# Performance work log

Hardware: AMD Instinct MI355X
Metric: run time of the kernel (lower is better)

Reference implementation:

```python
import jax, jax.numpy as jnp
import numpy as np

N = 200_000          # nodes
E = 12_800_000       # directed edges (avg degree 64)
C = 5                # channels: [pos_x, pos_y, vel_x, vel_y, extra]
ACCEL_SCALE = 0.01
MAX_VEL = 0.1
MAX_POS = 1.0


def setup_inputs() -> dict:
    key = jax.random.key(0)
    k1, k2, k3 = jax.random.split(key, 3)
    x = jax.random.uniform(k1, (N, C), jnp.float32, -1.0, 1.0)
    edge_index = jax.random.randint(k2, (2, E), 0, N, dtype=jnp.int32)
    # GCNConv learned params (glorot-ish init, zero bias as in PyG)
    W = jax.random.normal(k3, (C, 2), jnp.float32) * (1.0 / np.sqrt(C))
    b = jnp.zeros((2,), jnp.float32)
    return {"x": x, "edge_index": edge_index, "W": W, "b": b, "time_steps": 1}


def _gcn_conv(x, edge_index, W, b):
    """PyG GCNConv: add self-loops, symmetric deg normalization, X @ W, scatter-sum."""
    n = x.shape[0]
    loop = jnp.arange(n, dtype=edge_index.dtype)
    src = jnp.concatenate([edge_index[0], loop])  # [E+N]
    dst = jnp.concatenate([edge_index[1], loop])
    deg = jax.ops.segment_sum(jnp.ones_like(src, x.dtype), dst, num_segments=n)  # [N]
    dinv = jnp.where(deg > 0, jax.lax.rsqrt(deg), 0.0)
    norm = dinv[src] * dinv[dst]                  # [E+N]
    h = x @ W                                     # [N, 2]
    msg = h[src] * norm[:, None]                  # gather + scale, [E+N, 2]
    out = jax.ops.segment_sum(msg, dst, num_segments=n) + b
    return out


def _step(x, edge_index, W, b):
    acc = _gcn_conv(x, edge_index, W, b) * ACCEL_SCALE        # [N, 2]
    vel = jnp.clip(x[:, 2:4] + acc, -MAX_VEL, MAX_VEL)
    pos = jnp.clip(x[:, :2] + vel, -MAX_POS, MAX_POS)
    return jnp.concatenate([pos, vel, x[:, 4:]], axis=1)


def reference(x, edge_index, W, b, time_steps):
    for _ in range(time_steps):
        x = _step(x, edge_index, W, b)
    return x
```

## Files before the change

### kernel.cpp

```cpp
#include <hip/hip_runtime.h>
#include <hip/hip_fp16.h>

constexpr float ACCEL_SCALE = 0.01f;
constexpr float MAX_VEL = 0.1f;
constexpr float MAX_POS = 1.0f;

constexpr int GSHIFT = 11;
constexpr int GSIZE  = 1 << GSHIFT;
constexpr int SCANW  = 128;
constexpr int ANBLK  = 1024;
constexpr int DSHIFT = 4;
constexpr int ASHIFT = 5;

__global__ __launch_bounds__(256) void a_scatter_kernel(
    const int* __restrict__ src, const int* __restrict__ dst,
    int E, int NG, int chunk,
    unsigned* __restrict__ tab, unsigned* __restrict__ packed)
{
    __shared__ int cnt[SCANW];
    __shared__ int tmp[SCANW];
    __shared__ int cur[SCANW];
    int tid = threadIdx.x;
    long long cs64 = (long long)blockIdx.x * chunk;
    int cs = (cs64 > E) ? E : (int)cs64;
    int ce = min(cs + chunk, E);

    if (tid < SCANW) cnt[tid] = 0;
    __syncthreads();

    int nv = (ce - cs) >> 2;
    const int4* d4 = (const int4*)(dst + cs);
    for (int k = tid; k < nv; k += 256) {
        int4 v = d4[k];
        atomicAdd(&cnt[v.x >> GSHIFT], 1);
        atomicAdd(&cnt[v.y >> GSHIFT], 1);
        atomicAdd(&cnt[v.z >> GSHIFT], 1);
        atomicAdd(&cnt[v.w >> GSHIFT], 1);
    }
    for (int i = cs + (nv << 2) + tid; i < ce; i += 256)
        atomicAdd(&cnt[dst[i] >> GSHIFT], 1);
    __syncthreads();

    int v = (tid < SCANW) ? cnt[tid] : 0;
    if (tid < SCANW) tmp[tid] = v;
    __syncthreads();
    for (int off = 1; off < SCANW; off <<= 1) {
        int t = (tid < SCANW && tid >= off) ? tmp[tid - off] : 0;
        __syncthreads();
        if (tid < SCANW) tmp[tid] += t;
        __syncthreads();
    }
    if (tid < SCANW) {
        int base = tmp[tid] - v;
        cur[tid] = base;
        if (tid <= NG) tab[(size_t)blockIdx.x * (NG + 1) + tid] = (unsigned)base;
    }
    __syncthreads();

    const int4* s4 = (const int4*)(src + cs);
    for (int k = tid; k < nv; k += 256) {
        int4 dv = d4[k];
        int4 sv = s4[k];
        int p;
        p = atomicAdd(&cur[dv.x >> GSHIFT], 1);
        packed[cs + p] = ((unsigned)sv.x << GSHIFT) | (unsigned)(dv.x & (GSIZE - 1));
        p = atomicAdd(&cur[dv.y >> GSHIFT], 1);
        packed[cs + p] = ((unsigned)sv.y << GSHIFT) | (unsigned)(dv.y & (GSIZE - 1));
        p = atomicAdd(&cur[dv.z >> GSHIFT], 1);
        packed[cs + p] = ((unsigned)sv.z << GSHIFT) | (unsigned)(dv.z & (GSIZE - 1));
        p = atomicAdd(&cur[dv.w >> GSHIFT], 1);
        packed[cs + p] = ((unsigned)sv.w << GSHIFT) | (unsigned)(dv.w & (GSIZE - 1));
    }
    for (int i = cs + (nv << 2) + tid; i < ce; i += 256) {
        int dvv = dst[i], svv = src[i];
        int p = atomicAdd(&cur[dvv >> GSHIFT], 1);
        packed[cs + p] = ((unsigned)svv << GSHIFT) | (unsigned)(dvv & (GSIZE - 1));
    }
}

__global__ __launch_bounds__(512) void f_deg_kernel(
    const unsigned* __restrict__ packed, const unsigned* __restrict__ tab,
    int E, int NG, int chunk, int n, int splitShift, int* __restrict__ pdeg)
{
    __shared__ int cnt[GSIZE];
    int g = blockIdx.x >> splitShift;
    int s = blockIdx.x & ((1 << splitShift) - 1);
    for (int t = threadIdx.x; t < GSIZE; t += 512) cnt[t] = 0;
    __syncthreads();
    int wave = threadIdx.x >> 6, lane = threadIdx.x & 63;
    int perSplit = ANBLK >> splitShift;
    int j0 = s * perSplit, jend = j0 + perSplit;
    int j = j0 + wave;
    unsigned nt0 = 0, nt1 = 0;
    if (j < jend) { const unsigned* tr = tab + (size_t)j * (NG + 1) + g; nt0 = tr[0]; nt1 = tr[1]; }
    for (; j < jend; j += 8) {
        unsigned t0 = nt0, t1 = nt1;
        int jn = j + 8;
        if (jn < jend) { const unsigned* tr = tab + (size_t)jn * (NG + 1) + g; nt0 = tr[0]; nt1 = tr[1]; }
        long long cs64 = (long long)j * chunk;
        int cs = (cs64 > E) ? E : (int)cs64;
        for (unsigned i = t0 + lane; i < t1; i += 64)
            atomicAdd(&cnt[packed[cs + i] & (GSIZE - 1)], 1);
    }
    __syncthreads();
    size_t nb0 = (size_t)g << GSHIFT;
    for (int t = threadIdx.x; t < GSIZE; t += 512) {
        size_t node = nb0 + t;
        if (node < (size_t)n) pdeg[(size_t)s * n + node] = cnt[t];
    }
}

__global__ void node_preh_kernel(const float* __restrict__ x, const float* __restrict__ W,
                                 const int* __restrict__ pdeg, int n, int nsplit,
                                 float* __restrict__ dinv, __half2* __restrict__ hsh) {
    int i = blockIdx.x * blockDim.x + threadIdx.x;
    if (i >= n) return;
    int d = 1;
    for (int s = 0; s < nsplit; ++s) d += pdeg[(size_t)s * n + i];
    float di = rsqrtf((float)d);
    dinv[i] = di;
    const float* xr = x + (size_t)i * 5;
    float x0 = xr[0], x1 = xr[1], x2 = xr[2], x3 = xr[3], x4 = xr[4];
    float h0 = x0 * W[0] + x1 * W[2] + x2 * W[4] + x3 * W[6] + x4 * W[8];
    float h1 = x0 * W[1] + x1 * W[3] + x2 * W[5] + x3 * W[7] + x4 * W[9];
    hsh[i] = __floats2half2_rn(h0 * di, h1 * di);
}

__global__ __launch_bounds__(512) void a_acc5_kernel(
    const unsigned* __restrict__ packed, const unsigned* __restrict__ tab,
    const __half2* __restrict__ hsh, int E, int NG, int chunk, int n,
    __half2* __restrict__ psh)
{
    __shared__ __half2 acc[GSIZE];
    int g = blockIdx.x >> ASHIFT;
    int s = blockIdx.x & ((1 << ASHIFT) - 1);
    const __half2 zero = __floats2half2_rn(0.f, 0.f);
    for (int t = threadIdx.x; t < GSIZE; t += 512) acc[t] = zero;
    __syncthreads();
    int wave = threadIdx.x >> 6, lane = threadIdx.x & 63;
    const int perSplit = ANBLK >> ASHIFT;
    int j0 = s * perSplit, jend = j0 + perSplit;
    int j = j0 + wave;
    unsigned nt0 = 0, nt1 = 0;
    if (j < jend) { const unsigned* tr = tab + (size_t)j * (NG + 1) + g; nt0 = tr[0]; nt1 = tr[1]; }
    for (; j < jend; j += 8) {
        unsigned t0 = nt0, t1 = nt1;
        int jn = j + 8;
        if (jn < jend) { const unsigned* tr = tab + (size_t)jn * (NG + 1) + g; nt0 = tr[0]; nt1 = tr[1]; }
        long long cs64 = (long long)j * chunk;
        int cs = (cs64 > E) ? E : (int)cs64;
        for (unsigned i = t0 + lane; i < t1; i += 64) {
            unsigned p = packed[cs + i];
            __half2 m = hsh[p >> GSHIFT];
            unsafeAtomicAdd(&acc[p & (GSIZE - 1)], m);
        }
    }
    __syncthreads();
    size_t nb0 = (size_t)g << GSHIFT;
    for (int t = threadIdx.x; t < GSIZE; t += 512) {
        size_t node = nb0 + t;
        if (node < (size_t)n) psh[(size_t)s * n + node] = acc[t];
    }
}

__global__ void a_finalh_kernel(const float* __restrict__ x, const __half2* __restrict__ psh,
                                const float* __restrict__ W, const float* __restrict__ dinv,
                                const float* __restrict__ b, float* __restrict__ out,
                                int n, int nsplit) {
    int i = blockIdx.x * blockDim.x + threadIdx.x;
    if (i >= n) return;
    float sx = 0.f, sy = 0.f;
    for (int s = 0; s < nsplit; ++s) {
        float2 v = __half22float2(psh[(size_t)s * n + i]);
        sx += v.x; sy += v.y;
    }
    float di = dinv[i];
    const float* xr = x + (size_t)i * 5;
    float x0 = xr[0], x1 = xr[1], x2 = xr[2], x3 = xr[3], x4 = xr[4];
    float h0 = x0 * W[0] + x1 * W[2] + x2 * W[4] + x3 * W[6] + x4 * W[8];
    float h1 = x0 * W[1] + x1 * W[3] + x2 * W[5] + x3 * W[7] + x4 * W[9];
    float c0 = di * (sx + h0 * di) + b[0];
    float c1 = di * (sy + h1 * di) + b[1];
    float a0 = c0 * ACCEL_SCALE;
    float a1 = c1 * ACCEL_SCALE;
    float v0 = fminf(fmaxf(x2 + a0, -MAX_VEL), MAX_VEL);
    float v1 = fminf(fmaxf(x3 + a1, -MAX_VEL), MAX_VEL);
    float p0 = fminf(fmaxf(x0 + v0, -MAX_POS), MAX_POS);
    float p1 = fminf(fmaxf(x1 + v1, -MAX_POS), MAX_POS);
    float* o = out + (size_t)i * 5;
    o[0] = p0; o[1] = p1; o[2] = v0; o[3] = v1; o[4] = x4;
}

__global__ void node_pre_kernel(const float* __restrict__ x, const float* __restrict__ W,
                                const int* __restrict__ pdeg, int n, int nsplit,
                                float* __restrict__ dinv, float* __restrict__ hs) {
    int i = blockIdx.x * blockDim.x + threadIdx.x;
    if (i >= n) return;
    int d = 1;
    for (int s = 0; s < nsplit; ++s) d += pdeg[(size_t)s * n + i];
    float di = rsqrtf((float)d);
    dinv[i] = di;
    const float* xr = x + (size_t)i * 5;
    float x0 = xr[0], x1 = xr[1], x2 = xr[2], x3 = xr[3], x4 = xr[4];
    float h0 = x0 * W[0] + x1 * W[2] + x2 * W[4] + x3 * W[6] + x4 * W[8];
    float h1 = x0 * W[1] + x1 * W[3] + x2 * W[5] + x3 * W[7] + x4 * W[9];
    hs[2 * i]     = h0 * di;
    hs[2 * i + 1] = h1 * di;
}

__global__ __launch_bounds__(512) void f_acc_kernel(
    const unsigned* __restrict__ packed, const unsigned* __restrict__ tab,
    const float* __restrict__ hs, int E, int NG, int chunk, int n, int splitShift,
    float2* __restrict__ ps)
{
    __shared__ float accx[GSIZE];
    __shared__ float accy[GSIZE];
    int g = blockIdx.x >> splitShift;
    int s = blockIdx.x & ((1 << splitShift) - 1);
    for (int t = threadIdx.x; t < GSIZE; t += 512) { accx[t] = 0.f; accy[t] = 0.f; }
    __syncthreads();
    int wave = threadIdx.x >> 6, lane = threadIdx.x & 63;
    int perSplit = ANBLK >> splitShift;
    int j0 = s * perSplit, jend = j0 + perSplit;
    const float2* h2 = (const float2*)hs;
    int j = j0 + wave;
    unsigned nt0 = 0, nt1 = 0;
    if (j < jend) { const unsigned* tr = tab + (size_t)j * (NG + 1) + g; nt0 = tr[0]; nt1 = tr[1]; }
    for (; j < jend; j += 8) {
        unsigned t0 = nt0, t1 = nt1;
        int jn = j + 8;
        if (jn < jend) { const unsigned* tr = tab + (size_t)jn * (NG + 1) + g; nt0 = tr[0]; nt1 = tr[1]; }
        long long cs64 = (long long)j * chunk;
        int cs = (cs64 > E) ? E : (int)cs64;
        for (unsigned i = t0 + lane; i < t1; i += 64) {
            unsigned p = packed[cs + i];
            float2 m = h2[p >> GSHIFT];
            int ld = p & (GSIZE - 1);
            unsafeAtomicAdd(&accx[ld], m.x);
            unsafeAtomicAdd(&accy[ld], m.y);
        }
    }
    __syncthreads();
    size_t nb0 = (size_t)g << GSHIFT;
    for (int t = threadIdx.x; t < GSIZE; t += 512) {
        size_t node = nb0 + t;
        if (node < (size_t)n) ps[(size_t)s * n + node] = make_float2(accx[t], accy[t]);
    }
}

__global__ void a_final_kernel(const float* __restrict__ x, const float2* __restrict__ ps,
                               const float* __restrict__ hs, const float* __restrict__ dinv,
                               const float* __restrict__ b, float* __restrict__ out,
                               int n, int nsplit) {
    int i = blockIdx.x * blockDim.x + threadIdx.x;
    if (i >= n) return;
    float sx = 0.f, sy = 0.f;
    for (int s = 0; s < nsplit; ++s) {
        float2 v = ps[(size_t)s * n + i];
        sx += v.x; sy += v.y;
    }
    const float2* h2 = (const float2*)hs;
    float di = dinv[i];
    float2 hv = h2[i];
    float c0 = di * (sx + hv.x) + b[0];
    float c1 = di * (sy + hv.y) + b[1];
    float a0 = c0 * ACCEL_SCALE;
    float a1 = c1 * ACCEL_SCALE;
    const float* xr = x + (size_t)i * 5;
    float v0 = fminf(fmaxf(xr[2] + a0, -MAX_VEL), MAX_VEL);
    float v1 = fminf(fmaxf(xr[3] + a1, -MAX_VEL), MAX_VEL);
    float p0 = fminf(fmaxf(xr[0] + v0, -MAX_POS), MAX_POS);
    float p1 = fminf(fmaxf(xr[1] + v1, -MAX_POS), MAX_POS);
    float* o = out + (size_t)i * 5;
    o[0] = p0; o[1] = p1; o[2] = v0; o[3] = v1; o[4] = xr[4];
}

__global__ void fb_deg_kernel(const int* __restrict__ dst, int E, int* __restrict__ deg) {
    int tid = blockIdx.x * blockDim.x + threadIdx.x;
    int stride = gridDim.x * blockDim.x;
    for (int k = tid; k < E; k += stride) atomicAdd(&deg[dst[k]], 1);
}
__global__ void fb_scatter_kernel(const int* __restrict__ src, const int* __restrict__ dst,
                                  int E, const float* __restrict__ hs, float* __restrict__ s) {
    int tid = blockIdx.x * blockDim.x + threadIdx.x;
    int stride = gridDim.x * blockDim.x;
    const float2* h2 = (const float2*)hs;
    for (int k = tid; k < E; k += stride) {
        int sv = src[k], dv = dst[k];
        float2 m = h2[sv];
        unsafeAtomicAdd(&s[2 * dv], m.x);
        unsafeAtomicAdd(&s[2 * dv + 1], m.y);
    }
}
__global__ void fb_np_kernel(const float* __restrict__ x, const float* __restrict__ W,
                             const int* __restrict__ deg, int n,
                             float* __restrict__ dinv, float* __restrict__ hs) {
    int i = blockIdx.x * blockDim.x + threadIdx.x;
    if (i >= n) return;
    float di = rsqrtf((float)(deg[i] + 1));
    dinv[i] = di;
    const float* xr = x + (size_t)i * 5;
    float x0 = xr[0], x1 = xr[1], x2 = xr[2], x3 = xr[3], x4 = xr[4];
    float h0 = x0 * W[0] + x1 * W[2] + x2 * W[4] + x3 * W[6] + x4 * W[8];
    float h1 = x0 * W[1] + x1 * W[3] + x2 * W[5] + x3 * W[7] + x4 * W[9];
    hs[2 * i] = h0 * di;
    hs[2 * i + 1] = h1 * di;
}
__global__ void fb_finalize_kernel(const float* __restrict__ x, const float* __restrict__ s,
                                   const float* __restrict__ hs, const float* __restrict__ dinv,
                                   const float* __restrict__ b, float* __restrict__ out, int n) {
    int i = blockIdx.x * blockDim.x + threadIdx.x;
    if (i >= n) return;
    float di = dinv[i];
    const float2* s2 = (const float2*)s;
    const float2* h2 = (const float2*)hs;
    float2 sv = s2[i];
    float2 hv = h2[i];
    float c0 = di * (sv.x + hv.x) + b[0];
    float c1 = di * (sv.y + hv.y) + b[1];
    float a0 = c0 * ACCEL_SCALE, a1 = c1 * ACCEL_SCALE;
    const float* xr = x + (size_t)i * 5;
    float v0 = fminf(fmaxf(xr[2] + a0, -MAX_VEL), MAX_VEL);
    float v1 = fminf(fmaxf(xr[3] + a1, -MAX_VEL), MAX_VEL);
    float p0 = fminf(fmaxf(xr[0] + v0, -MAX_POS), MAX_POS);
    float p1 = fminf(fmaxf(xr[1] + v1, -MAX_POS), MAX_POS);
    float* o = out + (size_t)i * 5;
    o[0] = p0; o[1] = p1; o[2] = v0; o[3] = v1; o[4] = xr[4];
}

extern "C" void kernel_launch(void* const* d_in, const int* in_sizes, int n_in,
                              void* d_out, int out_size, void* d_ws, size_t ws_size,
                              hipStream_t stream) {
    const float* x    = (const float*)d_in[0];
    const int*   edge = (const int*)d_in[1];
    const float* W    = (const float*)d_in[2];
    const float* b    = (const float*)d_in[3];

    int n = in_sizes[0] / 5;
    int E = in_sizes[1] / 2;
    const int* src = edge;
    const int* dst = edge + E;

    const int BLK = 256;
    int node_blocks = (n + BLK - 1) / BLK;
    int NG = (n + GSIZE - 1) >> GSHIFT;
    int chunk = ((E + ANBLK - 1) / ANBLK + 3) & ~3;
    bool geomOK = (NG >= 1) && (NG + 1 <= SCANW) && (n <= (1 << 21)) && (E >= 8);

    if (geomOK) {
        const int dsplit = 1 << DSHIFT;
        const int asplit = 1 << ASHIFT;
        size_t wTab = (size_t)ANBLK * (NG + 1);
        size_t needW = (size_t)E + wTab + (size_t)dsplit * n + (size_t)asplit * n
                     + (size_t)n + (size_t)n;
        if (ws_size >= needW * 4) {
            unsigned* packed = (unsigned*)d_ws;
            unsigned* tab    = packed + E;
            int*      pdeg   = (int*)(tab + wTab);
            __half2*  psh    = (__half2*)(pdeg + (size_t)dsplit * n);
            float*    dinv   = (float*)(psh + (size_t)asplit * n);
            __half2*  hsh    = (__half2*)(dinv + n);

            a_scatter_kernel<<<ANBLK, 256, 0, stream>>>(src, dst, E, NG, chunk, tab, packed);
            f_deg_kernel<<<NG << DSHIFT, 512, 0, stream>>>(packed, tab, E, NG, chunk, n,
                                                           DSHIFT, pdeg);
            node_preh_kernel<<<node_blocks, BLK, 0, stream>>>(x, W, pdeg, n, dsplit, dinv, hsh);
            a_acc5_kernel<<<NG << ASHIFT, 512, 0, stream>>>(packed, tab, hsh, E, NG, chunk, n,
                                                            psh);
            a_finalh_kernel<<<node_blocks, BLK, 0, stream>>>(x, psh, W, dinv, b,
                                                             (float*)d_out, n, asplit);
            return;
        }
    }

    if (geomOK) {
        size_t baseW = (size_t)E + (size_t)ANBLK * (NG + 1) + (size_t)n + 2 * (size_t)n;
        size_t needF = (baseW + (size_t)4 * n * 2) * 4;
        if (ws_size >= needF) {
            const int splitShift = 2, split = 4;
            unsigned* packed = (unsigned*)d_ws;
            unsigned* tab    = packed + E;
            int* region      = (int*)(tab + (size_t)ANBLK * (NG + 1));
            int* pdeg        = region;
            float2* ps       = (float2*)region;
            float* dinv      = (float*)(region + (size_t)split * n * 2);
            float* hs        = dinv + n;

            a_scatter_kernel<<<ANBLK, 256, 0, stream>>>(src, dst, E, NG, chunk, tab, packed);
            f_deg_kernel<<<NG << splitShift, 512, 0, stream>>>(packed, tab, E, NG, chunk, n,
                                                               splitShift, pdeg);
            node_pre_kernel<<<node_blocks, BLK, 0, stream>>>(x, W, pdeg, n, split, dinv, hs);
            f_acc_kernel<<<NG << splitShift, 512, 0, stream>>>(packed, tab, hs, E, NG, chunk, n,
                                                               splitShift, ps);
            a_final_kernel<<<node_blocks, BLK, 0, stream>>>(x, ps, hs, dinv, b,
                                                            (float*)d_out, n, split);
            return;
        }
    }

    {
        float* dinv = (float*)d_ws;
        float* hs   = dinv + n;
        float* s    = hs + 2 * (size_t)n;
        int*   deg  = (int*)(s + 2 * (size_t)n);
        hipMemsetAsync(deg, 0, (size_t)n * sizeof(int), stream);
        hipMemsetAsync(s,   0, (size_t)n * 2 * sizeof(float), stream);
        fb_deg_kernel<<<4096, BLK, 0, stream>>>(dst, E, deg);
        fb_np_kernel<<<node_blocks, BLK, 0, stream>>>(x, W, deg, n, dinv, hs);
        fb_scatter_kernel<<<4096, BLK, 0, stream>>>(src, dst, E, hs, s);
        fb_finalize_kernel<<<node_blocks, BLK, 0, stream>>>(x, s, hs, dinv, b, (float*)d_out, n);
    }
}
```

Measured before the change: 173.9 us.

## Replace two-pass count-scan bucketing with single-pass fixed-capacity bins plus overflow list

The edge bucketing kernel no longer counts, scans and then scatters. Each block writes edges straight into fixed-capacity per-(block,group) slots, using a shared atomic cursor, and spills any excess into a global overflow list. Later kernels fix up the spilled edges with global atomics. This removes one full pass over the edge arrays and the scan, at the cost of a padded workspace, extra small kernels and a memset, and the overflow list is capped and silently drops edges past that cap.

New measurement: 178.9 us. 2.9% more time.

```diff
diff --git a/kernel.cpp b/kernel.cpp
--- a/kernel.cpp
+++ b/kernel.cpp
@@ -11,6 +11,190 @@
 constexpr int ANBLK  = 1024;
 constexpr int DSHIFT = 4;
 constexpr int ASHIFT = 5;
+constexpr int CAP    = 176;
+constexpr int OCAP   = 262144;
+
+
+__global__ __launch_bounds__(256) void n_scatter_kernel(
+    const int* __restrict__ src, const int* __restrict__ dst,
+    int E, int NG, int chunk,
+    unsigned* __restrict__ tabc, unsigned* __restrict__ packed,
+    unsigned* __restrict__ gofl, int2* __restrict__ ofl)
+{
+    __shared__ int cur[SCANW];
+    int tid = threadIdx.x;
+    long long cs64 = (long long)blockIdx.x * chunk;
+    int cs = (cs64 > E) ? E : (int)cs64;
+    int ce = min(cs + chunk, E);
+    if (tid < SCANW) cur[tid] = 0;
+    __syncthreads();
+
+    size_t obase = (size_t)blockIdx.x * NG;
+    int nv = (ce - cs) >> 2;
+    const int4* d4 = (const int4*)(dst + cs);
+    const int4* s4 = (const int4*)(src + cs);
+
+#define PROC(dd, ss)                                                            \
+    {                                                                           \
+        int b_ = (dd) >> GSHIFT;                                                \
+        int p_ = atomicAdd(&cur[b_], 1);                                        \
+        unsigned w_ = ((unsigned)(ss) << GSHIFT) | (unsigned)((dd) & (GSIZE-1));\
+        if (p_ < CAP) {                                                         \
+            packed[(obase + b_) * (size_t)CAP + p_] = w_;                       \
+        } else {                                                                \
+            unsigned op_ = atomicAdd(gofl, 1u);                                 \
+            if (op_ < (unsigned)OCAP) ofl[op_] = make_int2((ss), (dd));         \
+        }                                                                       \
+    }
+
+    for (int k = tid; k < nv; k += 256) {
+        int4 dv = d4[k];
+        int4 sv = s4[k];
+        PROC(dv.x, sv.x)
+        PROC(dv.y, sv.y)
+        PROC(dv.z, sv.z)
+        PROC(dv.w, sv.w)
+    }
+    for (int i = cs + (nv << 2) + tid; i < ce; i += 256) {
+        int dd = dst[i], ss = src[i];
+        PROC(dd, ss)
+    }
+#undef PROC
+    __syncthreads();
+    if (tid < NG) tabc[obase + tid] = (unsigned)min(cur[tid], CAP);
+}
+
+__global__ __launch_bounds__(512) void n_deg_kernel(
+    const unsigned* __restrict__ packed, const unsigned* __restrict__ tabc,
+    int NG, int n, int* __restrict__ pdeg)
+{
+    __shared__ int cnt[GSIZE];
+    int g = blockIdx.x >> DSHIFT;
+    int s = blockIdx.x & ((1 << DSHIFT) - 1);
+    for (int t = threadIdx.x; t < GSIZE; t += 512) cnt[t] = 0;
+    __syncthreads();
+    int wave = threadIdx.x >> 6, lane = threadIdx.x & 63;
+    const int perSplit = ANBLK >> DSHIFT;
+    int j0 = s * perSplit, jend = j0 + perSplit;
+    int j = j0 + wave;
+    unsigned nc = 0;
+    if (j < jend) nc = tabc[(size_t)j * NG + g];
+    for (; j < jend; j += 8) {
+        unsigned c = nc;
+        int jn = j + 8;
+        if (jn < jend) nc = tabc[(size_t)jn * NG + g];
+        size_t base = ((size_t)j * NG + g) * (size_t)CAP;
+        for (unsigned i = lane; i < c; i += 64)
+            atomicAdd(&cnt[packed[base + i] & (GSIZE - 1)], 1);
+    }
+    __syncthreads();
+    size_t nb0 = (size_t)g << GSHIFT;
+    for (int t = threadIdx.x; t < GSIZE; t += 512) {
+        size_t node = nb0 + t;
+        if (node < (size_t)n) pdeg[(size_t)s * n + node] = cnt[t];
+    }
+}
+
+__global__ void cln_deg_kernel(const unsigned* __restrict__ gofl, const int2* __restrict__ ofl,
+                               int* __restrict__ pdeg) {
+    unsigned oc = *gofl;
+    if (oc > (unsigned)OCAP) oc = OCAP;
+    for (unsigned k = blockIdx.x * blockDim.x + threadIdx.x; k < oc;
+         k += blockDim.x * gridDim.x)
+        atomicAdd(&pdeg[ofl[k].y], 1);
+}
+
+__global__ void node_preh_kernel(const float* __restrict__ x, const float* __restrict__ W,
+                                 const int* __restrict__ pdeg, int n, int nsplit,
+                                 float* __restrict__ dinv, __half2* __restrict__ hsh) {
+    int i = blockIdx.x * blockDim.x + threadIdx.x;
+    if (i >= n) return;
+    int d = 1;
+    for (int s = 0; s < nsplit; ++s) d += pdeg[(size_t)s * n + i];
+    float di = rsqrtf((float)d);
+    dinv[i] = di;
+    const float* xr = x + (size_t)i * 5;
+    float x0 = xr[0], x1 = xr[1], x2 = xr[2], x3 = xr[3], x4 = xr[4];
+    float h0 = x0 * W[0] + x1 * W[2] + x2 * W[4] + x3 * W[6] + x4 * W[8];
+    float h1 = x0 * W[1] + x1 * W[3] + x2 * W[5] + x3 * W[7] + x4 * W[9];
+    hsh[i] = __floats2half2_rn(h0 * di, h1 * di);
+}
+
+__global__ __launch_bounds__(512) void n_acc_kernel(
+    const unsigned* __restrict__ packed, const unsigned* __restrict__ tabc,
+    const __half2* __restrict__ hsh, int NG, int n,
+    __half2* __restrict__ psh)
+{
+    __shared__ __half2 acc[GSIZE];
+    int g = blockIdx.x >> ASHIFT;
+    int s = blockIdx.x & ((1 << ASHIFT) - 1);
+    const __half2 zero = __floats2half2_rn(0.f, 0.f);
+    for (int t = threadIdx.x; t < GSIZE; t += 512) acc[t] = zero;
+    __syncthreads();
+    int wave = threadIdx.x >> 6, lane = threadIdx.x & 63;
+    const int perSplit = ANBLK >> ASHIFT;
+    int j0 = s * perSplit, jend = j0 + perSplit;
+    int j = j0 + wave;
+    unsigned nc = 0;
+    if (j < jend) nc = tabc[(size_t)j * NG + g];
+    for (; j < jend; j += 8) {
+        unsigned c = nc;
+        int jn = j + 8;
+        if (jn < jend) nc = tabc[(size_t)jn * NG + g];
+        size_t base = ((size_t)j * NG + g) * (size_t)CAP;
+        for (unsigned i = lane; i < c; i += 64) {
+            unsigned p = packed[base + i];
+            __half2 m = hsh[p >> GSHIFT];
+            unsafeAtomicAdd(&acc[p & (GSIZE - 1)], m);
+        }
+    }
+    __syncthreads();
+    size_t nb0 = (size_t)g << GSHIFT;
+    for (int t = threadIdx.x; t < GSIZE; t += 512) {
+        size_t node = nb0 + t;
+        if (node < (size_t)n) psh[(size_t)s * n + node] = acc[t];
+    }
+}
+
+__global__ void cln_acc_kernel(const unsigned* __restrict__ gofl, const int2* __restrict__ ofl,
+                               const __half2* __restrict__ hsh, __half2* __restrict__ psh) {
+    unsigned oc = *gofl;
+    if (oc > (unsigned)OCAP) oc = OCAP;
+    for (unsigned k = blockIdx.x * blockDim.x + threadIdx.x; k < oc;
+         k += blockDim.x * gridDim.x) {
+        int2 e = ofl[k];
+        unsafeAtomicAdd(&psh[e.y], hsh[e.x]);
+    }
+}
+
+__global__ void a_finalh_kernel(const float* __restrict__ x, const __half2* __restrict__ psh,
+                                const float* __restrict__ W, const float* __restrict__ dinv,
+                                const float* __restrict__ b, float* __restrict__ out,
+                                int n, int nsplit) {
+    int i = blockIdx.x * blockDim.x + threadIdx.x;
+    if (i >= n) return;
+    float sx = 0.f, sy = 0.f;
+    for (int s = 0; s < nsplit; ++s) {
+        float2 v = __half22float2(psh[(size_t)s * n + i]);
+        sx += v.x; sy += v.y;
+    }
+    float di = dinv[i];
+    const float* xr = x + (size_t)i * 5;
+    float x0 = xr[0], x1 = xr[1], x2 = xr[2], x3 = xr[3], x4 = xr[4];
+    float h0 = x0 * W[0] + x1 * W[2] + x2 * W[4] + x3 * W[6] + x4 * W[8];
+    float h1 = x0 * W[1] + x1 * W[3] + x2 * W[5] + x3 * W[7] + x4 * W[9];
+    float c0 = di * (sx + h0 * di) + b[0];
+    float c1 = di * (sy + h1 * di) + b[1];
+    float a0 = c0 * ACCEL_SCALE;
+    float a1 = c1 * ACCEL_SCALE;
+    float v0 = fminf(fmaxf(x2 + a0, -MAX_VEL), MAX_VEL);
+    float v1 = fminf(fmaxf(x3 + a1, -MAX_VEL), MAX_VEL);
+    float p0 = fminf(fmaxf(x0 + v0, -MAX_POS), MAX_POS);
+    float p1 = fminf(fmaxf(x1 + v1, -MAX_POS), MAX_POS);
+    float* o = out + (size_t)i * 5;
+    o[0] = p0; o[1] = p1; o[2] = v0; o[3] = v1; o[4] = x4;
+}
+
 
 __global__ __launch_bounds__(256) void a_scatter_kernel(
     const int* __restrict__ src, const int* __restrict__ dst,
@@ -108,22 +292,6 @@
         size_t node = nb0 + t;
         if (node < (size_t)n) pdeg[(size_t)s * n + node] = cnt[t];
     }
-}
-
-__global__ void node_preh_kernel(const float* __restrict__ x, const float* __restrict__ W,
-                                 const int* __restrict__ pdeg, int n, int nsplit,
-                                 float* __restrict__ dinv, __half2* __restrict__ hsh) {
-    int i = blockIdx.x * blockDim.x + threadIdx.x;
-    if (i >= n) return;
-    int d = 1;
-    for (int s = 0; s < nsplit; ++s) d += pdeg[(size_t)s * n + i];
-    float di = rsqrtf((float)d);
-    dinv[i] = di;
-    const float* xr = x + (size_t)i * 5;
-    float x0 = xr[0], x1 = xr[1], x2 = xr[2], x3 = xr[3], x4 = xr[4];
-    float h0 = x0 * W[0] + x1 * W[2] + x2 * W[4] + x3 * W[6] + x4 * W[8];
-    float h1 = x0 * W[1] + x1 * W[3] + x2 * W[5] + x3 * W[7] + x4 * W[9];
-    hsh[i] = __floats2half2_rn(h0 * di, h1 * di);
 }
 
 __global__ __launch_bounds__(512) void a_acc5_kernel(
@@ -161,118 +329,6 @@
         size_t node = nb0 + t;
         if (node < (size_t)n) psh[(size_t)s * n + node] = acc[t];
     }
-}
-
-__global__ void a_finalh_kernel(const float* __restrict__ x, const __half2* __restrict__ psh,
-                                const float* __restrict__ W, const float* __restrict__ dinv,
-                                const float* __restrict__ b, float* __restrict__ out,
-                                int n, int nsplit) {
-    int i = blockIdx.x * blockDim.x + threadIdx.x;
-    if (i >= n) return;
-    float sx = 0.f, sy = 0.f;
-    for (int s = 0; s < nsplit; ++s) {
-        float2 v = __half22float2(psh[(size_t)s * n + i]);
-        sx += v.x; sy += v.y;
-    }
-    float di = dinv[i];
-    const float* xr = x + (size_t)i * 5;
-    float x0 = xr[0], x1 = xr[1], x2 = xr[2], x3 = xr[3], x4 = xr[4];
-    float h0 = x0 * W[0] + x1 * W[2] + x2 * W[4] + x3 * W[6] + x4 * W[8];
-    float h1 = x0 * W[1] + x1 * W[3] + x2 * W[5] + x3 * W[7] + x4 * W[9];
-    float c0 = di * (sx + h0 * di) + b[0];
-    float c1 = di * (sy + h1 * di) + b[1];
-    float a0 = c0 * ACCEL_SCALE;
-    float a1 = c1 * ACCEL_SCALE;
-    float v0 = fminf(fmaxf(x2 + a0, -MAX_VEL), MAX_VEL);
-    float v1 = fminf(fmaxf(x3 + a1, -MAX_VEL), MAX_VEL);
-    float p0 = fminf(fmaxf(x0 + v0, -MAX_POS), MAX_POS);
-    float p1 = fminf(fmaxf(x1 + v1, -MAX_POS), MAX_POS);
-    float* o = out + (size_t)i * 5;
-    o[0] = p0; o[1] = p1; o[2] = v0; o[3] = v1; o[4] = x4;
-}
-
-__global__ void node_pre_kernel(const float* __restrict__ x, const float* __restrict__ W,
-                                const int* __restrict__ pdeg, int n, int nsplit,
-                                float* __restrict__ dinv, float* __restrict__ hs) {
-    int i = blockIdx.x * blockDim.x + threadIdx.x;
-    if (i >= n) return;
-    int d = 1;
-    for (int s = 0; s < nsplit; ++s) d += pdeg[(size_t)s * n + i];
-    float di = rsqrtf((float)d);
-    dinv[i] = di;
-    const float* xr = x + (size_t)i * 5;
-    float x0 = xr[0], x1 = xr[1], x2 = xr[2], x3 = xr[3], x4 = xr[4];
-    float h0 = x0 * W[0] + x1 * W[2] + x2 * W[4] + x3 * W[6] + x4 * W[8];
-    float h1 = x0 * W[1] + x1 * W[3] + x2 * W[5] + x3 * W[7] + x4 * W[9];
-    hs[2 * i]     = h0 * di;
-    hs[2 * i + 1] = h1 * di;
-}
-
-__global__ __launch_bounds__(512) void f_acc_kernel(
-    const unsigned* __restrict__ packed, const unsigned* __restrict__ tab,
-    const float* __restrict__ hs, int E, int NG, int chunk, int n, int splitShift,
-    float2* __restrict__ ps)
-{
-    __shared__ float accx[GSIZE];
-    __shared__ float accy[GSIZE];
-    int g = blockIdx.x >> splitShift;
-    int s = blockIdx.x & ((1 << splitShift) - 1);
-    for (int t = threadIdx.x; t < GSIZE; t += 512) { accx[t] = 0.f; accy[t] = 0.f; }
-    __syncthreads();
-    int wave = threadIdx.x >> 6, lane = threadIdx.x & 63;
-    int perSplit = ANBLK >> splitShift;
-    int j0 = s * perSplit, jend = j0 + perSplit;
-    const float2* h2 = (const float2*)hs;
-    int j = j0 + wave;
-    unsigned nt0 = 0, nt1 = 0;
-    if (j < jend) { const unsigned* tr = tab + (size_t)j * (NG + 1) + g; nt0 = tr[0]; nt1 = tr[1]; }
-    for (; j < jend; j += 8) {
-        unsigned t0 = nt0, t1 = nt1;
-        int jn = j + 8;
-        if (jn < jend) { const unsigned* tr = tab + (size_t)jn * (NG + 1) + g; nt0 = tr[0]; nt1 = tr[1]; }
-        long long cs64 = (long long)j * chunk;
-        int cs = (cs64 > E) ? E : (int)cs64;
-        for (unsigned i = t0 + lane; i < t1; i += 64) {
-            unsigned p = packed[cs + i];
-            float2 m = h2[p >> GSHIFT];
-            int ld = p & (GSIZE - 1);
-            unsafeAtomicAdd(&accx[ld], m.x);
-            unsafeAtomicAdd(&accy[ld], m.y);
-        }
-    }
-    __syncthreads();
-    size_t nb0 = (size_t)g << GSHIFT;
-    for (int t = threadIdx.x; t < GSIZE; t += 512) {
-        size_t node = nb0 + t;
-        if (node < (size_t)n) ps[(size_t)s * n + node] = make_float2(accx[t], accy[t]);
-    }
-}
-
-__global__ void a_final_kernel(const float* __restrict__ x, const float2* __restrict__ ps,
-                               const float* __restrict__ hs, const float* __restrict__ dinv,
-                               const float* __restrict__ b, float* __restrict__ out,
-                               int n, int nsplit) {
-    int i = blockIdx.x * blockDim.x + threadIdx.x;
-    if (i >= n) return;
-    float sx = 0.f, sy = 0.f;
-    for (int s = 0; s < nsplit; ++s) {
-        float2 v = ps[(size_t)s * n + i];
-        sx += v.x; sy += v.y;
-    }
-    const float2* h2 = (const float2*)hs;
-    float di = dinv[i];
-    float2 hv = h2[i];
-    float c0 = di * (sx + hv.x) + b[0];
-    float c1 = di * (sy + hv.y) + b[1];
-    float a0 = c0 * ACCEL_SCALE;
-    float a1 = c1 * ACCEL_SCALE;
-    const float* xr = x + (size_t)i * 5;
-    float v0 = fminf(fmaxf(xr[2] + a0, -MAX_VEL), MAX_VEL);
-    float v1 = fminf(fmaxf(xr[3] + a1, -MAX_VEL), MAX_VEL);
-    float p0 = fminf(fmaxf(xr[0] + v0, -MAX_POS), MAX_POS);
-    float p1 = fminf(fmaxf(xr[1] + v1, -MAX_POS), MAX_POS);
-    float* o = out + (size_t)i * 5;
-    o[0] = p0; o[1] = p1; o[2] = v0; o[3] = v1; o[4] = xr[4];
 }
 
 __global__ void fb_deg_kernel(const int* __restrict__ dst, int E, int* __restrict__ deg) {
@@ -345,15 +401,44 @@
     int node_blocks = (n + BLK - 1) / BLK;
     int NG = (n + GSIZE - 1) >> GSHIFT;
     int chunk = ((E + ANBLK - 1) / ANBLK + 3) & ~3;
-    bool geomOK = (NG >= 1) && (NG + 1 <= SCANW) && (n <= (1 << 21)) && (E >= 8);
-
-    if (geomOK) {
-        const int dsplit = 1 << DSHIFT;
-        const int asplit = 1 << ASHIFT;
+    const int dsplit = 1 << DSHIFT;
+    const int asplit = 1 << ASHIFT;
+    bool geomOK = (NG >= 1) && (NG <= SCANW) && (n <= (1 << 21)) && (E >= 8);
+
+    if (geomOK && NG + 1 <= SCANW) {
+        size_t cells = (size_t)ANBLK * NG;
+        size_t needN = 16 + cells * CAP + cells + (size_t)2 * OCAP
+                     + (size_t)asplit * n + (size_t)n + (size_t)n;
+        if (ws_size >= needN * 4) {
+            unsigned* gofl   = (unsigned*)d_ws;
+            unsigned* packed = gofl + 16;
+            unsigned* tabc   = packed + cells * CAP;
+            int2*     ofl    = (int2*)(tabc + cells);
+            int*      region = (int*)(ofl + OCAP);
+            int*      pdeg   = region;
+            __half2*  psh    = (__half2*)region;
+            float*    dinv   = (float*)(region + (size_t)asplit * n);
+            __half2*  hsh    = (__half2*)(dinv + n);
+
+            hipMemsetAsync(gofl, 0, 64, stream);
+            n_scatter_kernel<<<ANBLK, 256, 0, stream>>>(src, dst, E, NG, chunk,
+                                                        tabc, packed, gofl, ofl);
+            n_deg_kernel<<<NG << DSHIFT, 512, 0, stream>>>(packed, tabc, NG, n, pdeg);
+            cln_deg_kernel<<<4, 256, 0, stream>>>(gofl, ofl, pdeg);
+            node_preh_kernel<<<node_blocks, BLK, 0, stream>>>(x, W, pdeg, n, dsplit, dinv, hsh);
+            n_acc_kernel<<<NG << ASHIFT, 512, 0, stream>>>(packed, tabc, hsh, NG, n, psh);
+            cln_acc_kernel<<<4, 256, 0, stream>>>(gofl, ofl, hsh, psh);
+            a_finalh_kernel<<<node_blocks, BLK, 0, stream>>>(x, psh, W, dinv, b,
+                                                             (float*)d_out, n, asplit);
+            return;
+        }
+    }
+
+    if (geomOK && NG + 1 <= SCANW) {
         size_t wTab = (size_t)ANBLK * (NG + 1);
-        size_t needW = (size_t)E + wTab + (size_t)dsplit * n + (size_t)asplit * n
+        size_t needF = (size_t)E + wTab + (size_t)dsplit * n + (size_t)asplit * n
                      + (size_t)n + (size_t)n;
-        if (ws_size >= needW * 4) {
+        if (ws_size >= needF * 4) {
             unsigned* packed = (unsigned*)d_ws;
             unsigned* tab    = packed + E;
             int*      pdeg   = (int*)(tab + wTab);
@@ -369,31 +454,6 @@
                                                             psh);
             a_finalh_kernel<<<node_blocks, BLK, 0, stream>>>(x, psh, W, dinv, b,
                                                              (float*)d_out, n, asplit);
-            return;
-        }
-    }
-
-    if (geomOK) {
-        size_t baseW = (size_t)E + (size_t)ANBLK * (NG + 1) + (size_t)n + 2 * (size_t)n;
-        size_t needF = (baseW + (size_t)4 * n * 2) * 4;
-        if (ws_size >= needF) {
-            const int splitShift = 2, split = 4;
-            unsigned* packed = (unsigned*)d_ws;
-            unsigned* tab    = packed + E;
-            int* region      = (int*)(tab + (size_t)ANBLK * (NG + 1));
-            int* pdeg        = region;
-            float2* ps       = (float2*)region;
-            float* dinv      = (float*)(region + (size_t)split * n * 2);
-            float* hs        = dinv + n;
-
-            a_scatter_kernel<<<ANBLK, 256, 0, stream>>>(src, dst, E, NG, chunk, tab, packed);
-            f_deg_kernel<<<NG << splitShift, 512, 0, stream>>>(packed, tab, E, NG, chunk, n,
-                                                               splitShift, pdeg);
-            node_pre_kernel<<<node_blocks, BLK, 0, stream>>>(x, W, pdeg, n, split, dinv, hs);
-            f_acc_kernel<<<NG << splitShift, 512, 0, stream>>>(packed, tab, hs, E, NG, chunk, n,
-                                                               splitShift, ps);
-            a_final_kernel<<<node_blocks, BLK, 0, stream>>>(x, ps, hs, dinv, b,
-                                                            (float*)d_out, n, split);
             return;
         }
     }
```

## Replace shared atomic bucket counting with per-thread histograms and deterministic scan

Applied to the files above, without the earlier changes.

Adds a partition kernel in which each thread keeps its own 16-bit bucket counters in LDS, replacing shared-memory atomics during both the counting and the placement passes. Per-bucket prefix sums over the thread histograms give each thread fixed write offsets, so placement within a chunk becomes deterministic and atomic-free. The cost is a large LDS footprint (about 50KB) that limits occupancy, a serial 128-step scan per bucket, and loss of int4-vectorised loads. The older fp32 fallback path is removed and the original scatter is kept only when the group count exceeds the padding.

Measured after the change: 294.4 us. 1.69x slower.

```diff
diff --git a/kernel.cpp b/kernel.cpp
--- a/kernel.cpp
+++ b/kernel.cpp
@@ -8,41 +8,55 @@
 constexpr int GSHIFT = 11;
 constexpr int GSIZE  = 1 << GSHIFT;
 constexpr int SCANW  = 128;
+constexpr int BPAD   = 100;
 constexpr int ANBLK  = 1024;
 constexpr int DSHIFT = 4;
 constexpr int ASHIFT = 5;
 
-__global__ __launch_bounds__(256) void a_scatter_kernel(
+
+__global__ __launch_bounds__(256) void p_scatter_kernel(
     const int* __restrict__ src, const int* __restrict__ dst,
     int E, int NG, int chunk,
     unsigned* __restrict__ tab, unsigned* __restrict__ packed)
 {
-    __shared__ int cnt[SCANW];
+    __shared__ unsigned short cnt[256][BPAD];
+    __shared__ unsigned halfTot[BPAD][2];
+    __shared__ int bbase[SCANW];
     __shared__ int tmp[SCANW];
-    __shared__ int cur[SCANW];
     int tid = threadIdx.x;
     long long cs64 = (long long)blockIdx.x * chunk;
     int cs = (cs64 > E) ? E : (int)cs64;
     int ce = min(cs + chunk, E);
-
-    if (tid < SCANW) cnt[tid] = 0;
-    __syncthreads();
-
-    int nv = (ce - cs) >> 2;
-    const int4* d4 = (const int4*)(dst + cs);
-    for (int k = tid; k < nv; k += 256) {
-        int4 v = d4[k];
-        atomicAdd(&cnt[v.x >> GSHIFT], 1);
-        atomicAdd(&cnt[v.y >> GSHIFT], 1);
-        atomicAdd(&cnt[v.z >> GSHIFT], 1);
-        atomicAdd(&cnt[v.w >> GSHIFT], 1);
-    }
-    for (int i = cs + (nv << 2) + tid; i < ce; i += 256)
-        atomicAdd(&cnt[dst[i] >> GSHIFT], 1);
-    __syncthreads();
-
-    int v = (tid < SCANW) ? cnt[tid] : 0;
-    if (tid < SCANW) tmp[tid] = v;
+    int len = ce - cs;
+
+    unsigned* cz = (unsigned*)&cnt[0][0];
+    for (int i = tid; i < 256 * BPAD / 2; i += 256) cz[i] = 0;
+    __syncthreads();
+
+    for (int k = tid; k < len; k += 256) {
+        int b = dst[cs + k] >> GSHIFT;
+        cnt[tid][b] = (unsigned short)(cnt[tid][b] + 1);
+    }
+    __syncthreads();
+
+    if (tid < 2 * NG) {
+        int b = tid >> 1, half = tid & 1;
+        int t0 = half << 7;
+        unsigned run = 0;
+        for (int i = 0; i < 128; ++i) {
+            unsigned v = cnt[t0 + i][b];
+            cnt[t0 + i][b] = (unsigned short)run;
+            run += v;
+        }
+        halfTot[b][half] = run;
+    }
+    __syncthreads();
+
+    int v = 0;
+    if (tid < SCANW) {
+        v = (tid < NG) ? (int)(halfTot[tid][0] + halfTot[tid][1]) : 0;
+        tmp[tid] = v;
+    }
     __syncthreads();
     for (int off = 1; off < SCANW; off <<= 1) {
         int t = (tid < SCANW && tid >= off) ? tmp[tid - off] : 0;
@@ -52,29 +66,18 @@
     }
     if (tid < SCANW) {
         int base = tmp[tid] - v;
-        cur[tid] = base;
+        bbase[tid] = base;
         if (tid <= NG) tab[(size_t)blockIdx.x * (NG + 1) + tid] = (unsigned)base;
     }
     __syncthreads();
 
-    const int4* s4 = (const int4*)(src + cs);
-    for (int k = tid; k < nv; k += 256) {
-        int4 dv = d4[k];
-        int4 sv = s4[k];
-        int p;
-        p = atomicAdd(&cur[dv.x >> GSHIFT], 1);
-        packed[cs + p] = ((unsigned)sv.x << GSHIFT) | (unsigned)(dv.x & (GSIZE - 1));
-        p = atomicAdd(&cur[dv.y >> GSHIFT], 1);
-        packed[cs + p] = ((unsigned)sv.y << GSHIFT) | (unsigned)(dv.y & (GSIZE - 1));
-        p = atomicAdd(&cur[dv.z >> GSHIFT], 1);
-        packed[cs + p] = ((unsigned)sv.z << GSHIFT) | (unsigned)(dv.z & (GSIZE - 1));
-        p = atomicAdd(&cur[dv.w >> GSHIFT], 1);
-        packed[cs + p] = ((unsigned)sv.w << GSHIFT) | (unsigned)(dv.w & (GSIZE - 1));
-    }
-    for (int i = cs + (nv << 2) + tid; i < ce; i += 256) {
-        int dvv = dst[i], svv = src[i];
-        int p = atomicAdd(&cur[dvv >> GSHIFT], 1);
-        packed[cs + p] = ((unsigned)svv << GSHIFT) | (unsigned)(dvv & (GSIZE - 1));
+    for (int k = tid; k < len; k += 256) {
+        int dd = dst[cs + k], ss = src[cs + k];
+        int b = dd >> GSHIFT;
+        unsigned r = cnt[tid][b];
+        cnt[tid][b] = (unsigned short)(r + 1);
+        int p = bbase[b] + (int)r + (int)((tid >> 7) ? halfTot[b][0] : 0u);
+        packed[cs + p] = ((unsigned)ss << GSHIFT) | (unsigned)(dd & (GSIZE - 1));
     }
 }
 
@@ -191,88 +194,71 @@
     o[0] = p0; o[1] = p1; o[2] = v0; o[3] = v1; o[4] = x4;
 }
 
-__global__ void node_pre_kernel(const float* __restrict__ x, const float* __restrict__ W,
-                                const int* __restrict__ pdeg, int n, int nsplit,
-                                float* __restrict__ dinv, float* __restrict__ hs) {
-    int i = blockIdx.x * blockDim.x + threadIdx.x;
-    if (i >= n) return;
-    int d = 1;
-    for (int s = 0; s < nsplit; ++s) d += pdeg[(size_t)s * n + i];
-    float di = rsqrtf((float)d);
-    dinv[i] = di;
-    const float* xr = x + (size_t)i * 5;
-    float x0 = xr[0], x1 = xr[1], x2 = xr[2], x3 = xr[3], x4 = xr[4];
-    float h0 = x0 * W[0] + x1 * W[2] + x2 * W[4] + x3 * W[6] + x4 * W[8];
-    float h1 = x0 * W[1] + x1 * W[3] + x2 * W[5] + x3 * W[7] + x4 * W[9];
-    hs[2 * i]     = h0 * di;
-    hs[2 * i + 1] = h1 * di;
-}
-
-__global__ __launch_bounds__(512) void f_acc_kernel(
-    const unsigned* __restrict__ packed, const unsigned* __restrict__ tab,
-    const float* __restrict__ hs, int E, int NG, int chunk, int n, int splitShift,
-    float2* __restrict__ ps)
+
+__global__ __launch_bounds__(256) void a_scatter_kernel(
+    const int* __restrict__ src, const int* __restrict__ dst,
+    int E, int NG, int chunk,
+    unsigned* __restrict__ tab, unsigned* __restrict__ packed)
 {
-    __shared__ float accx[GSIZE];
-    __shared__ float accy[GSIZE];
-    int g = blockIdx.x >> splitShift;
-    int s = blockIdx.x & ((1 << splitShift) - 1);
-    for (int t = threadIdx.x; t < GSIZE; t += 512) { accx[t] = 0.f; accy[t] = 0.f; }
-    __syncthreads();
-    int wave = threadIdx.x >> 6, lane = threadIdx.x & 63;
-    int perSplit = ANBLK >> splitShift;
-    int j0 = s * perSplit, jend = j0 + perSplit;
-    const float2* h2 = (const float2*)hs;
-    int j = j0 + wave;
-    unsigned nt0 = 0, nt1 = 0;
-    if (j < jend) { const unsigned* tr = tab + (size_t)j * (NG + 1) + g; nt0 = tr[0]; nt1 = tr[1]; }
-    for (; j < jend; j += 8) {
-        unsigned t0 = nt0, t1 = nt1;
-        int jn = j + 8;
-        if (jn < jend) { const unsigned* tr = tab + (size_t)jn * (NG + 1) + g; nt0 = tr[0]; nt1 = tr[1]; }
-        long long cs64 = (long long)j * chunk;
-        int cs = (cs64 > E) ? E : (int)cs64;
-        for (unsigned i = t0 + lane; i < t1; i += 64) {
-            unsigned p = packed[cs + i];
-            float2 m = h2[p >> GSHIFT];
-            int ld = p & (GSIZE - 1);
-            unsafeAtomicAdd(&accx[ld], m.x);
-            unsafeAtomicAdd(&accy[ld], m.y);
-        }
-    }
-    __syncthreads();
-    size_t nb0 = (size_t)g << GSHIFT;
-    for (int t = threadIdx.x; t < GSIZE; t += 512) {
-        size_t node = nb0 + t;
-        if (node < (size_t)n) ps[(size_t)s * n + node] = make_float2(accx[t], accy[t]);
-    }
-}
-
-__global__ void a_final_kernel(const float* __restrict__ x, const float2* __restrict__ ps,
-                               const float* __restrict__ hs, const float* __restrict__ dinv,
-                               const float* __restrict__ b, float* __restrict__ out,
-                               int n, int nsplit) {
-    int i = blockIdx.x * blockDim.x + threadIdx.x;
-    if (i >= n) return;
-    float sx = 0.f, sy = 0.f;
-    for (int s = 0; s < nsplit; ++s) {
-        float2 v = ps[(size_t)s * n + i];
-        sx += v.x; sy += v.y;
-    }
-    const float2* h2 = (const float2*)hs;
-    float di = dinv[i];
-    float2 hv = h2[i];
-    float c0 = di * (sx + hv.x) + b[0];
-    float c1 = di * (sy + hv.y) + b[1];
-    float a0 = c0 * ACCEL_SCALE;
-    float a1 = c1 * ACCEL_SCALE;
-    const float* xr = x + (size_t)i * 5;
-    float v0 = fminf(fmaxf(xr[2] + a0, -MAX_VEL), MAX_VEL);
-    float v1 = fminf(fmaxf(xr[3] + a1, -MAX_VEL), MAX_VEL);
-    float p0 = fminf(fmaxf(xr[0] + v0, -MAX_POS), MAX_POS);
-    float p1 = fminf(fmaxf(xr[1] + v1, -MAX_POS), MAX_POS);
-    float* o = out + (size_t)i * 5;
-    o[0] = p0; o[1] = p1; o[2] = v0; o[3] = v1; o[4] = xr[4];
+    __shared__ int cnt[SCANW];
+    __shared__ int tmp[SCANW];
+    __shared__ int cur[SCANW];
+    int tid = threadIdx.x;
+    long long cs64 = (long long)blockIdx.x * chunk;
+    int cs = (cs64 > E) ? E : (int)cs64;
+    int ce = min(cs + chunk, E);
+
+    if (tid < SCANW) cnt[tid] = 0;
+    __syncthreads();
+
+    int nv = (ce - cs) >> 2;
+    const int4* d4 = (const int4*)(dst + cs);
+    for (int k = tid; k < nv; k += 256) {
+        int4 v = d4[k];
+        atomicAdd(&cnt[v.x >> GSHIFT], 1);
+        atomicAdd(&cnt[v.y >> GSHIFT], 1);
+        atomicAdd(&cnt[v.z >> GSHIFT], 1);
+        atomicAdd(&cnt[v.w >> GSHIFT], 1);
+    }
+    for (int i = cs + (nv << 2) + tid; i < ce; i += 256)
+        atomicAdd(&cnt[dst[i] >> GSHIFT], 1);
+    __syncthreads();
+
+    int v = (tid < SCANW) ? cnt[tid] : 0;
+    if (tid < SCANW) tmp[tid] = v;
+    __syncthreads();
+    for (int off = 1; off < SCANW; off <<= 1) {
+        int t = (tid < SCANW && tid >= off) ? tmp[tid - off] : 0;
+        __syncthreads();
+        if (tid < SCANW) tmp[tid] += t;
+        __syncthreads();
+    }
+    if (tid < SCANW) {
+        int base = tmp[tid] - v;
+        cur[tid] = base;
+        if (tid <= NG) tab[(size_t)blockIdx.x * (NG + 1) + tid] = (unsigned)base;
+    }
+    __syncthreads();
+
+    const int4* s4 = (const int4*)(src + cs);
+    for (int k = tid; k < nv; k += 256) {
+        int4 dv = d4[k];
+        int4 sv = s4[k];
+        int p;
+        p = atomicAdd(&cur[dv.x >> GSHIFT], 1);
+        packed[cs + p] = ((unsigned)sv.x << GSHIFT) | (unsigned)(dv.x & (GSIZE - 1));
+        p = atomicAdd(&cur[dv.y >> GSHIFT], 1);
+        packed[cs + p] = ((unsigned)sv.y << GSHIFT) | (unsigned)(dv.y & (GSIZE - 1));
+        p = atomicAdd(&cur[dv.z >> GSHIFT], 1);
+        packed[cs + p] = ((unsigned)sv.z << GSHIFT) | (unsigned)(dv.z & (GSIZE - 1));
+        p = atomicAdd(&cur[dv.w >> GSHIFT], 1);
+        packed[cs + p] = ((unsigned)sv.w << GSHIFT) | (unsigned)(dv.w & (GSIZE - 1));
+    }
+    for (int i = cs + (nv << 2) + tid; i < ce; i += 256) {
+        int dvv = dst[i], svv = src[i];
+        int p = atomicAdd(&cur[dvv >> GSHIFT], 1);
+        packed[cs + p] = ((unsigned)svv << GSHIFT) | (unsigned)(dvv & (GSIZE - 1));
+    }
 }
 
 __global__ void fb_deg_kernel(const int* __restrict__ dst, int E, int* __restrict__ deg) {
@@ -345,57 +331,50 @@
     int node_blocks = (n + BLK - 1) / BLK;
     int NG = (n + GSIZE - 1) >> GSHIFT;
     int chunk = ((E + ANBLK - 1) / ANBLK + 3) & ~3;
+    const int dsplit = 1 << DSHIFT;
+    const int asplit = 1 << ASHIFT;
     bool geomOK = (NG >= 1) && (NG + 1 <= SCANW) && (n <= (1 << 21)) && (E >= 8);
 
-    if (geomOK) {
-        const int dsplit = 1 << DSHIFT;
-        const int asplit = 1 << ASHIFT;
-        size_t wTab = (size_t)ANBLK * (NG + 1);
-        size_t needW = (size_t)E + wTab + (size_t)dsplit * n + (size_t)asplit * n
-                     + (size_t)n + (size_t)n;
-        if (ws_size >= needW * 4) {
-            unsigned* packed = (unsigned*)d_ws;
-            unsigned* tab    = packed + E;
-            int*      pdeg   = (int*)(tab + wTab);
-            __half2*  psh    = (__half2*)(pdeg + (size_t)dsplit * n);
-            float*    dinv   = (float*)(psh + (size_t)asplit * n);
-            __half2*  hsh    = (__half2*)(dinv + n);
-
-            a_scatter_kernel<<<ANBLK, 256, 0, stream>>>(src, dst, E, NG, chunk, tab, packed);
-            f_deg_kernel<<<NG << DSHIFT, 512, 0, stream>>>(packed, tab, E, NG, chunk, n,
-                                                           DSHIFT, pdeg);
-            node_preh_kernel<<<node_blocks, BLK, 0, stream>>>(x, W, pdeg, n, dsplit, dinv, hsh);
-            a_acc5_kernel<<<NG << ASHIFT, 512, 0, stream>>>(packed, tab, hsh, E, NG, chunk, n,
-                                                            psh);
-            a_finalh_kernel<<<node_blocks, BLK, 0, stream>>>(x, psh, W, dinv, b,
-                                                             (float*)d_out, n, asplit);
-            return;
-        }
-    }
-
-    if (geomOK) {
-        size_t baseW = (size_t)E + (size_t)ANBLK * (NG + 1) + (size_t)n + 2 * (size_t)n;
-        size_t needF = (baseW + (size_t)4 * n * 2) * 4;
-        if (ws_size >= needF) {
-            const int splitShift = 2, split = 4;
-            unsigned* packed = (unsigned*)d_ws;
-            unsigned* tab    = packed + E;
-            int* region      = (int*)(tab + (size_t)ANBLK * (NG + 1));
-            int* pdeg        = region;
-            float2* ps       = (float2*)region;
-            float* dinv      = (float*)(region + (size_t)split * n * 2);
-            float* hs        = dinv + n;
-
-            a_scatter_kernel<<<ANBLK, 256, 0, stream>>>(src, dst, E, NG, chunk, tab, packed);
-            f_deg_kernel<<<NG << splitShift, 512, 0, stream>>>(packed, tab, E, NG, chunk, n,
-                                                               splitShift, pdeg);
-            node_pre_kernel<<<node_blocks, BLK, 0, stream>>>(x, W, pdeg, n, split, dinv, hs);
-            f_acc_kernel<<<NG << splitShift, 512, 0, stream>>>(packed, tab, hs, E, NG, chunk, n,
-                                                               splitShift, ps);
-            a_final_kernel<<<node_blocks, BLK, 0, stream>>>(x, ps, hs, dinv, b,
-                                                            (float*)d_out, n, split);
-            return;
-        }
+    size_t wTab = (size_t)ANBLK * (NG + 1);
+    size_t needW = (size_t)E + wTab + (size_t)dsplit * n + (size_t)asplit * n
+                 + (size_t)n + (size_t)n;
+
+    if (geomOK && NG <= BPAD && ws_size >= needW * 4) {
+        unsigned* packed = (unsigned*)d_ws;
+        unsigned* tab    = packed + E;
+        int*      pdeg   = (int*)(tab + wTab);
+        __half2*  psh    = (__half2*)(pdeg + (size_t)dsplit * n);
+        float*    dinv   = (float*)(psh + (size_t)asplit * n);
+        __half2*  hsh    = (__half2*)(dinv + n);
+
+        p_scatter_kernel<<<ANBLK, 256, 0, stream>>>(src, dst, E, NG, chunk, tab, packed);
+        f_deg_kernel<<<NG << DSHIFT, 512, 0, stream>>>(packed, tab, E, NG, chunk, n,
+                                                       DSHIFT, pdeg);
+        node_preh_kernel<<<node_blocks, BLK, 0, stream>>>(x, W, pdeg, n, dsplit, dinv, hsh);
+        a_acc5_kernel<<<NG << ASHIFT, 512, 0, stream>>>(packed, tab, hsh, E, NG, chunk, n,
+                                                        psh);
+        a_finalh_kernel<<<node_blocks, BLK, 0, stream>>>(x, psh, W, dinv, b,
+                                                         (float*)d_out, n, asplit);
+        return;
+    }
+
+    if (geomOK && ws_size >= needW * 4) {
+        unsigned* packed = (unsigned*)d_ws;
+        unsigned* tab    = packed + E;
+        int*      pdeg   = (int*)(tab + wTab);
+        __half2*  psh    = (__half2*)(pdeg + (size_t)dsplit * n);
+        float*    dinv   = (float*)(psh + (size_t)asplit * n);
+        __half2*  hsh    = (__half2*)(dinv + n);
+
+        a_scatter_kernel<<<ANBLK, 256, 0, stream>>>(src, dst, E, NG, chunk, tab, packed);
+        f_deg_kernel<<<NG << DSHIFT, 512, 0, stream>>>(packed, tab, E, NG, chunk, n,
+                                                       DSHIFT, pdeg);
+        node_preh_kernel<<<node_blocks, BLK, 0, stream>>>(x, W, pdeg, n, dsplit, dinv, hsh);
+        a_acc5_kernel<<<NG << ASHIFT, 512, 0, stream>>>(packed, tab, hsh, E, NG, chunk, n,
+                                                        psh);
+        a_finalh_kernel<<<node_blocks, BLK, 0, stream>>>(x, psh, W, dinv, b,
+                                                         (float*)d_out, n, asplit);
+        return;
     }
 
     {
```
